# Kernel tuning notes

Measured on AMD Instinct MI355X. Metric: run time of the kernel, lower is better.

## Reference

```python
import jax, jax.numpy as jnp
import numpy as np

N, E, D, F = 8192, 262144, 256, 512  # nodes, edges, hidden_dim, ffn hidden
M = 256  # performer num_random_features (default)


def _ln(x, g, b, eps=1e-5):
    mu = jnp.mean(x, axis=-1, keepdims=True)
    var = jnp.mean((x - mu) ** 2, axis=-1, keepdims=True)
    return (x - mu) * jax.lax.rsqrt(var + eps) * g + b


def setup_inputs() -> dict:
    key = jax.random.key(0)
    ks = jax.random.split(key, 16)
    s = 1.0 / np.sqrt(D)
    return {
        "h": jax.random.normal(ks[0], (N, D), dtype=jnp.float32),
        "edge_index": jax.random.randint(ks[1], (2, E), 0, N, dtype=jnp.int32),
        "W_gcn": jax.random.normal(ks[2], (D, D), dtype=jnp.float32) * s,
        "b_gcn": jnp.zeros((D,), jnp.float32),
        "Wq": jax.random.normal(ks[3], (D, D), dtype=jnp.float32) * s,
        "bq": jnp.zeros((D,), jnp.float32),
        "Wk": jax.random.normal(ks[4], (D, D), dtype=jnp.float32) * s,
        "bk": jnp.zeros((D,), jnp.float32),
        "Wv": jax.random.normal(ks[5], (D, D), dtype=jnp.float32) * s,
        "bv": jnp.zeros((D,), jnp.float32),
        "Wo": jax.random.normal(ks[6], (D, D), dtype=jnp.float32) * s,
        "bo": jnp.zeros((D,), jnp.float32),
        "RF": jax.random.normal(ks[7], (M, D), dtype=jnp.float32) * s,  # random feature projection
        "g1": jnp.ones((D,), jnp.float32), "be1": jnp.zeros((D,), jnp.float32),
        "g2": jnp.ones((D,), jnp.float32), "be2": jnp.zeros((D,), jnp.float32),
        "g3": jnp.ones((D,), jnp.float32), "be3": jnp.zeros((D,), jnp.float32),
        "W1": jax.random.normal(ks[8], (D, F), dtype=jnp.float32) * s,
        "b1": jnp.zeros((F,), jnp.float32),
        "W2": jax.random.normal(ks[9], (F, D), dtype=jnp.float32) * (1.0 / np.sqrt(F)),
        "b2": jnp.zeros((D,), jnp.float32),
    }


def _gps_forward(h, edge_index, W_gcn, b_gcn, Wq, bq, Wk, bk, Wv, bv, Wo, bo, RF,
                 g1, be1, g2, be2, g3, be3, W1, b1, W2, b2):
    n = h.shape[0]
    # ---- local GCNConv (add self loops, symmetric norm) ----
    loops = jnp.arange(n, dtype=edge_index.dtype)
    src = jnp.concatenate([edge_index[0], loops])
    dst = jnp.concatenate([edge_index[1], loops])
    deg = jax.ops.segment_sum(jnp.ones_like(src, dtype=h.dtype), dst, num_segments=n)
    dinv = jnp.where(deg > 0, jax.lax.rsqrt(jnp.maximum(deg, 1e-12)), 0.0)
    coef = dinv[src] * dinv[dst]  # [E+N]
    xw = h @ W_gcn  # [N, D]
    h_local = jax.ops.segment_sum(xw[src] * coef[:, None], dst, num_segments=n) + b_gcn
    h1 = _ln(h + h_local, g1, be1)  # dropout p applied in train only; eval here
    # ---- global Performer attention (as written: dense NxN in feature space) ----
    q = h1 @ Wq + bq
    k = h1 @ Wk + bk
    v = h1 @ Wv + bv
    qf = q @ RF.T  # [N, M]
    kf = k @ RF.T  # [N, M]
    scores = (qf @ kf.T) / jnp.sqrt(jnp.asarray(h.shape[-1], h.dtype))  # [N, N]
    attw = jax.nn.softmax(scores, axis=-1)
    h_global = (attw @ v) @ Wo + bo
    h2 = _ln(h1 + h_global, g2, be2)
    # ---- FFN ----
    h_ffn = jnp.maximum(h2 @ W1 + b1, 0.0) @ W2 + b2
    return _ln(h2 + h_ffn, g3, be3)


def reference(h, edge_index, W_gcn, b_gcn, Wq, bq, Wk, bk, Wv, bv, Wo, bo, RF,
              g1, be1, g2, be2, g3, be3, W1, b1, W2, b2):
    return _gps_forward(h, edge_index, W_gcn, b_gcn, Wq, bq, Wk, bk, Wv, bv, Wo, bo, RF,
                        g1, be1, g2, be2, g3, be3, W1, b1, W2, b2)
```

## Files before the change

### kernel.cpp

```cpp
#include <hip/hip_runtime.h>
#include <hip/hip_bf16.h>

#define NN 8192
#define EE 262144
#define DD 256
#define FF 512
#define MM 256

typedef __attribute__((ext_vector_type(8))) short short8v;
typedef __attribute__((ext_vector_type(16))) float float16v;

__device__ __forceinline__ ushort f2bf(float x) {
  union { float f; unsigned u; } c; c.f = x;
  unsigned r = (c.u + 0x7FFF + ((c.u >> 16) & 1)) >> 16;
  return (ushort)r;
}
__device__ __forceinline__ float b2f(ushort u) {
  union { unsigned u; float f; } c; c.u = ((unsigned)u) << 16;
  return c.f;
}
__device__ __forceinline__ void async_copy16(void* lds, const void* g) {
  __builtin_amdgcn_global_load_lds(
      (const __attribute__((address_space(1))) void*)g,
      (__attribute__((address_space(3))) void*)lds, 16, 0, 0);
}

__global__ __launch_bounds__(1024) void scan_kernel(const int* __restrict__ degi,
                                                    int* __restrict__ csr_off,
                                                    float* __restrict__ dinv) {
  __shared__ int part[1024];
  int tid = threadIdx.x;
  int base = tid * 8;
  int loc[8], dv[8]; int s = 0;
#pragma unroll
  for (int i = 0; i < 8; ++i) { int d = degi[base + i]; dv[i] = d; loc[i] = s; s += d; }
  part[tid] = s;
  __syncthreads();
  for (int off = 1; off < 1024; off <<= 1) {
    int v = (tid >= off) ? part[tid - off] : 0;
    __syncthreads();
    part[tid] += v;
    __syncthreads();
  }
  int pre = (tid == 0) ? 0 : part[tid - 1];
#pragma unroll
  for (int i = 0; i < 8; ++i) {
    csr_off[base + i] = pre + loc[i];
    dinv[base + i] = rsqrtf((float)(dv[i] + 1));
  }
  if (tid == 1023) csr_off[NN] = part[1023];
}

__global__ void fill_kernel(const int* __restrict__ ei, const int* __restrict__ csr_off,
                            int* __restrict__ cursor, int* __restrict__ csr_src) {
  int i = blockIdx.x * blockDim.x + threadIdx.x;
  if (i < EE) {
    int d = ei[EE + i];
    int pos = csr_off[d] + atomicAdd(&cursor[d], 1);
    csr_src[pos] = ei[i];
  }
}

#define QSCALE 0.090168441f
#define P1B 10753
__global__ __launch_bounds__(256) void prep_kernel(
    const float* __restrict__ h, const float* __restrict__ W_gcn,
    const float* __restrict__ Wv, const float* __restrict__ Wo,
    const float* __restrict__ W1, const float* __restrict__ W2,
    const float* __restrict__ bv,
    const float* __restrict__ Wq, const float* __restrict__ Wk,
    const float* __restrict__ bq, const float* __restrict__ bk,
    const float* __restrict__ RF, const int* __restrict__ ei,
    ushort* __restrict__ hb, ushort* __restrict__ WgcnT, ushort* __restrict__ Wcat,
    ushort* __restrict__ WoT, ushort* __restrict__ W1T, ushort* __restrict__ W2T,
    ushort* __restrict__ RFb, ushort* __restrict__ Wqkb,
    float* __restrict__ bcat, int* __restrict__ degi)
{
  if (blockIdx.x < P1B) {
    int i = blockIdx.x * 256 + threadIdx.x;
    const int R0 = NN * DD;
    const int R1 = R0 + DD * DD;
    const int R2 = R1 + DD * DD;
    const int R3 = R2 + DD * DD;
    const int R4 = R3 + DD * FF;
    const int R5 = R4 + FF * DD;
    const int R6 = R5 + DD;
    const int R7 = R6 + DD * DD;
    const int R8 = R7 + DD * DD;
    const int R9 = R8 + DD * DD;
    if (i < R0) {
      hb[i] = f2bf(h[i]);
    } else if (i < R1) {
      int j = i - R0; int n = j >> 8, k = j & 255;
      WgcnT[(n << 8) | k] = f2bf(W_gcn[k * DD + n]);
    } else if (i < R2) {
      int j = i - R1; int n = j >> 8, k = j & 255;
      Wcat[((512 + n) << 8) | k] = f2bf(Wv[k * DD + n]);
    } else if (i < R3) {
      int j = i - R2; int n = j >> 8, k = j & 255;
      WoT[(n << 8) | k] = f2bf(Wo[k * DD + n]);
    } else if (i < R4) {
      int j = i - R3; int n = j >> 8, k = j & 255;
      W1T[(n << 8) | k] = f2bf(W1[k * FF + n]);
    } else if (i < R5) {
      int j = i - R4; int n = j >> 9, k = j & 511;
      W2T[n * FF + k] = f2bf(W2[k * DD + n]);
    } else if (i < R6) {
      bcat[512 + (i - R5)] = bv[i - R5];
    } else if (i < R7) {
      int j = i - R6;
      RFb[j] = f2bf(RF[j]);
    } else if (i < R8) {
      int j = i - R7;
      Wqkb[j] = f2bf(Wq[j] * QSCALE);
    } else if (i < R9) {
      int j = i - R8;
      Wqkb[DD * DD + j] = f2bf(Wk[j]);
    }
  } else if (blockIdx.x < P1B + 2) {
    const int b = blockIdx.x - P1B;
    const int m = threadIdx.x;
    const float* bvec = (b == 0) ? bq : bk;
    const float alpha = (b == 0) ? QSCALE : 1.0f;
    float s = 0.0f;
    for (int j = 0; j < DD; ++j) s = fmaf(bvec[j], RF[m * DD + j], s);
    bcat[(b == 0 ? 0 : 256) + m] = s * alpha;
  } else {
    int i = (blockIdx.x - P1B - 2) * 256 + threadIdx.x;
    if (i < EE) atomicAdd(&degi[ei[EE + i]], 1);
  }
}

template<int OMODE, bool RELU>
__global__ __launch_bounds__(512) void gemm_bf16_kernel(
    const ushort* __restrict__ A, const ushort* __restrict__ BT,
    const float* __restrict__ bias, void* __restrict__ Cv,
    void* __restrict__ Cv2, void* __restrict__ Cv3,
    int M, int N, int K)
{
  __shared__ ushort As[2][4096];
  __shared__ ushort Bs[2][4096];
  const int tid = threadIdx.x;
  const int c32 = tid & 31, hi = (tid >> 5) & 1;
  const int wv = tid >> 6;
  const int q = wv & 3, ks = wv >> 2;
  const int qm = (q >> 1) << 5, qn = (q & 1) << 5;
  const int m0 = blockIdx.y * 64, n0 = blockIdx.x * 64;

  const int sr = tid >> 3, spsl = tid & 7;
  const int ssl = spsl ^ ((sr >> 2) & 7);
  const ushort* Asrc = A + (size_t)(m0 + sr) * K + (ssl << 3);
  const ushort* Bsrc = BT + (size_t)(n0 + sr) * K + (ssl << 3);

  const int ra = qm + c32, rb = qn + c32;
  const int ga = (ra >> 2) & 7, gb = (rb >> 2) & 7;

  float16v acc = (float16v)(0.0f);

#define GS(b, k0) { \
    async_copy16(&As[b][tid << 3], Asrc + (k0)); \
    async_copy16(&Bs[b][tid << 3], Bsrc + (k0)); }

  GS(0, 0)
  const int nk = K >> 6;
  for (int kt = 0; kt < nk; ++kt) {
    asm volatile("s_waitcnt vmcnt(0)" ::: "memory");
    __syncthreads();
    if (kt + 1 < nk) GS((kt + 1) & 1, (kt + 1) << 6)
    const ushort* as_ = As[kt & 1];
    const ushort* bs_ = Bs[kt & 1];
    __builtin_amdgcn_s_setprio(1);
#pragma unroll
    for (int k2 = 0; k2 < 2; ++k2) {
      const int k16 = (ks << 1) + k2;
      const int sl = (k16 << 1) + hi;
      short8v af = *(const short8v*)&as_[(ra << 6) + ((sl ^ ga) << 3)];
      short8v bf = *(const short8v*)&bs_[(rb << 6) + ((sl ^ gb) << 3)];
      acc = __builtin_amdgcn_mfma_f32_32x32x16_bf16(af, bf, acc, 0, 0, 0);
    }
    __builtin_amdgcn_s_setprio(0);
  }
#undef GS

  __syncthreads();
  float* red = (float*)&As[0][0];
  if (ks == 1) {
#pragma unroll
    for (int r = 0; r < 16; ++r) {
      const int crow = (r & 3) + ((r >> 2) << 3) + (hi << 2);
      red[(q << 10) + (crow << 5) + c32] = acc[r];
    }
  }
  __syncthreads();
  if (ks == 0) {
    const int col = n0 + qn + c32;
    const float bv = bias ? bias[col] : 0.0f;
    if (OMODE == 3 && col >= 512) {
#pragma unroll
      for (int g = 0; g < 4; ++g) {
        float v0 = acc[g * 4 + 0] + red[(q << 10) + (((0) + (g << 3) + (hi << 2)) << 5) + c32] + bv;
        float v1 = acc[g * 4 + 1] + red[(q << 10) + (((1) + (g << 3) + (hi << 2)) << 5) + c32] + bv;
        float v2 = acc[g * 4 + 2] + red[(q << 10) + (((2) + (g << 3) + (hi << 2)) << 5) + c32] + bv;
        float v3 = acc[g * 4 + 3] + red[(q << 10) + (((3) + (g << 3) + (hi << 2)) << 5) + c32] + bv;
        ushort4 o; o.x = f2bf(v0); o.y = f2bf(v1); o.z = f2bf(v2); o.w = f2bf(v3);
        *(ushort4*)&((ushort*)Cv3)[(size_t)(col - 512) * NN + m0 + qm + (g << 3) + (hi << 2)] = o;
      }
    } else {
#pragma unroll
      for (int r = 0; r < 16; ++r) {
        const int crow = (r & 3) + ((r >> 2) << 3) + (hi << 2);
        const int m = m0 + qm + crow;
        float v = acc[r] + red[(q << 10) + (crow << 5) + c32] + bv;
        if (RELU) v = fmaxf(v, 0.0f);
        if (OMODE == 4) {
          ((ushort*)Cv)[(size_t)m * N + col] = f2bf(v);
        } else if (OMODE == 5) {
          if (col < 256) ((ushort*)Cv)[(size_t)m * 256 + col] = f2bf(v);
          else ((ushort*)Cv)[(size_t)(256 + m) * 256 + (col - 256)] = f2bf(v);
        } else {
          if (col < 256) {
            ((ushort*)Cv)[(size_t)m * 256 + col] = f2bf(v);
          } else {
            const int c2 = (col - 256) ^ ((m & 7) << 3) ^ (((m >> 3) & 3) << 6);
            ((ushort*)Cv2)[(size_t)m * 256 + c2] = f2bf(v);
          }
        }
      }
    }
  }
}

__global__ __launch_bounds__(256) void gcn_gather_ln_kernel(
    const ushort* __restrict__ xwb, const float* __restrict__ h,
    const float* __restrict__ dinv, const int* __restrict__ csr_off,
    const int* __restrict__ csr_src, const float* __restrict__ b_gcn,
    const float* __restrict__ g1, const float* __restrict__ be1,
    float* __restrict__ h1, ushort* __restrict__ h1b)
{
  const int node = blockIdx.x * 4 + (threadIdx.x >> 6);
  const int t = threadIdx.x & 63;
  const int c4 = t << 2;
  const float di = dinv[node];
  const int e0 = csr_off[node], e1 = csr_off[node + 1];
  float acc[4] = {0.f, 0.f, 0.f, 0.f};
  for (int e = e0; e < e1; ++e) {
    int s = csr_src[e];
    float ds = dinv[s];
    ushort4 xv = *(const ushort4*)&xwb[(size_t)s * DD + c4];
    acc[0] = fmaf(b2f(xv.x), ds, acc[0]);
    acc[1] = fmaf(b2f(xv.y), ds, acc[1]);
    acc[2] = fmaf(b2f(xv.z), ds, acc[2]);
    acc[3] = fmaf(b2f(xv.w), ds, acc[3]);
  }
  ushort4 sv = *(const ushort4*)&xwb[(size_t)node * DD + c4];
  float4 hv = *(const float4*)&h[(size_t)node * DD + c4];
  float4 bg = *(const float4*)&b_gcn[c4];
  const float dii = di * di;
  float y[4];
  y[0] = fmaf(acc[0], di, b2f(sv.x) * dii) + bg.x + hv.x;
  y[1] = fmaf(acc[1], di, b2f(sv.y) * dii) + bg.y + hv.y;
  y[2] = fmaf(acc[2], di, b2f(sv.z) * dii) + bg.z + hv.z;
  y[3] = fmaf(acc[3], di, b2f(sv.w) * dii) + bg.w + hv.w;
  float s1 = (y[0] + y[1]) + (y[2] + y[3]);
  float s2 = (y[0]*y[0] + y[1]*y[1]) + (y[2]*y[2] + y[3]*y[3]);
#pragma unroll
  for (int m = 1; m <= 32; m <<= 1) { s1 += __shfl_xor(s1, m); s2 += __shfl_xor(s2, m); }
  float mu = s1 * (1.0f / 256.0f);
  float var = s2 * (1.0f / 256.0f) - mu * mu;
  float inv = rsqrtf(fmaxf(var, 0.0f) + 1e-5f);
  float4 g4 = *(const float4*)&g1[c4];
  float4 b4 = *(const float4*)&be1[c4];
  float v0 = (y[0] - mu) * inv * g4.x + b4.x;
  float v1 = (y[1] - mu) * inv * g4.y + b4.y;
  float v2 = (y[2] - mu) * inv * g4.z + b4.z;
  float v3 = (y[3] - mu) * inv * g4.w + b4.w;
  *(float4*)&h1[(size_t)node * DD + c4] = make_float4(v0, v1, v2, v3);
  ushort4 ob; ob.x = f2bf(v0); ob.y = f2bf(v1); ob.z = f2bf(v2); ob.w = f2bf(v3);
  *(ushort4*)&h1b[(node << 8) + c4] = ob;
}

__global__ __launch_bounds__(256, 2) void flash_mfma_kernel(
    const ushort* __restrict__ qb, const ushort* __restrict__ kb,
    const ushort* __restrict__ vbT, ushort* __restrict__ opb,
    float* __restrict__ ml, int ksn, int kchunk)
{
  __shared__ ushort Kbuf[2][8192];
  __shared__ ushort Vbuf[2][8192];

  const int tid = threadIdx.x;
  const int l = tid & 63, wv = tid >> 6;
  const int c32 = l & 31, hi = l >> 5;
  const int qt = blockIdx.x / ksn, ks = blockIdx.x % ksn;
  const int q0 = qt * 128;
  const int kbase = ks * kchunk;

  const int vrow = tid >> 2;
  const ushort* kptr = kb + (size_t)(kbase + (tid >> 5)) * 256 + ((tid & 31) << 3);
  const ushort* vptr = vbT + (size_t)vrow * NN + kbase + (((tid & 3) ^ ((vrow >> 3) & 3)) << 3);

#define FSTAGE(b) { \
    _Pragma("unroll") \
    for (int c = 0; c < 4; ++c) { \
      async_copy16(&Kbuf[b][((c << 8) + tid) << 3], kptr + (size_t)c * (8 * 256)); \
      async_copy16(&Vbuf[b][((c << 8) + tid) << 3], vptr + (size_t)c * (64 * NN)); \
    } }

  FSTAGE(0)

  short8v qfr[16];
  {
    const ushort* qrow = qb + (size_t)(q0 + wv * 32 + c32) * 256 + (hi << 3);
#pragma unroll
    for (int kk = 0; kk < 16; ++kk)
      qfr[kk] = *(const short8v*)(qrow + (kk << 4));
  }

  float16v acc[8];
#pragma unroll
  for (int dt = 0; dt < 8; ++dt) acc[dt] = (float16v)(0.0f);
  float lsum = 0.f;

  const int ksw = ((c32 & 7) << 3) | (((c32 >> 3) & 3) << 6);
  const int vsw = (c32 >> 3) & 3;
  const int voff0 = (hi ^ vsw) << 3;
  const int voff1 = ((2 + hi) ^ vsw) << 3;

  const int nit = kchunk >> 5;
  for (int it = 0; it < nit; ++it) {
    asm volatile("s_waitcnt vmcnt(0)" ::: "memory");
    __syncthreads();
    if (it + 1 < nit) {
      kptr += 32 * 256;
      vptr += 32;
      FSTAGE((it + 1) & 1)
    }
    const ushort* Kp = Kbuf[it & 1];
    const ushort* Vp = Vbuf[it & 1];

    float16v s = (float16v)(0.0f);
    __builtin_amdgcn_s_setprio(1);
#pragma unroll
    for (int kk = 0; kk < 16; ++kk) {
      short8v kf = *(const short8v*)&Kp[(c32 << 8) + (((kk << 4) + (hi << 3)) ^ ksw)];
      s = __builtin_amdgcn_mfma_f32_32x32x16_bf16(kf, qfr[kk], s, 0, 0, 0);
    }
    __builtin_amdgcn_s_setprio(0);

    float p[16];
#pragma unroll
    for (int r = 0; r < 16; ++r) p[r] = exp2f(s[r]);
    {
      float t0 = (p[0] + p[1]) + (p[2] + p[3]);
      float t1 = (p[4] + p[5]) + (p[6] + p[7]);
      float t2 = (p[8] + p[9]) + (p[10] + p[11]);
      float t3 = (p[12] + p[13]) + (p[14] + p[15]);
      lsum += (t0 + t1) + (t2 + t3);
    }
    unsigned u0, u1, u2, u3, u4, u5, u6, u7;
    asm("v_cvt_pk_bf16_f32 %0, %1, %2" : "=v"(u0) : "v"(p[0]),  "v"(p[1]));
    asm("v_cvt_pk_bf16_f32 %0, %1, %2" : "=v"(u1) : "v"(p[2]),  "v"(p[3]));
    asm("v_cvt_pk_bf16_f32 %0, %1, %2" : "=v"(u2) : "v"(p[4]),  "v"(p[5]));
    asm("v_cvt_pk_bf16_f32 %0, %1, %2" : "=v"(u3) : "v"(p[6]),  "v"(p[7]));
    asm("v_cvt_pk_bf16_f32 %0, %1, %2" : "=v"(u4) : "v"(p[8]),  "v"(p[9]));
    asm("v_cvt_pk_bf16_f32 %0, %1, %2" : "=v"(u5) : "v"(p[10]), "v"(p[11]));
    asm("v_cvt_pk_bf16_f32 %0, %1, %2" : "=v"(u6) : "v"(p[12]), "v"(p[13]));
    asm("v_cvt_pk_bf16_f32 %0, %1, %2" : "=v"(u7) : "v"(p[14]), "v"(p[15]));
    asm volatile("v_permlane32_swap_b32 %0, %1" : "+v"(u0), "+v"(u2));
    asm volatile("v_permlane32_swap_b32 %0, %1" : "+v"(u1), "+v"(u3));
    asm volatile("v_permlane32_swap_b32 %0, %1" : "+v"(u4), "+v"(u6));
    asm volatile("v_permlane32_swap_b32 %0, %1" : "+v"(u5), "+v"(u7));
    union { unsigned uu[4]; short8v v; } P0, P1;
    P0.uu[0] = u0; P0.uu[1] = u1; P0.uu[2] = u2; P0.uu[3] = u3;
    P1.uu[0] = u4; P1.uu[1] = u5; P1.uu[2] = u6; P1.uu[3] = u7;

    __builtin_amdgcn_s_setprio(1);
#pragma unroll
    for (int dt = 0; dt < 8; ++dt) {
      const int drow = (dt << 5) + c32;
      short8v vf0 = *(const short8v*)&Vp[(drow << 5) + voff0];
      short8v vf1 = *(const short8v*)&Vp[(drow << 5) + voff1];
      acc[dt] = __builtin_amdgcn_mfma_f32_32x32x16_bf16(P0.v, vf0, acc[dt], 0, 0, 0);
      acc[dt] = __builtin_amdgcn_mfma_f32_32x32x16_bf16(P1.v, vf1, acc[dt], 0, 0, 0);
    }
    __builtin_amdgcn_s_setprio(0);
  }
#undef FSTAGE

  float lt = lsum + __shfl_xor(lsum, 32);
  if (hi == 0) ml[(size_t)ks * NN + q0 + wv * 32 + c32] = lt;
  ushort* op = opb + (size_t)ks * (NN * DD);
#pragma unroll
  for (int dt = 0; dt < 8; ++dt)
#pragma unroll
    for (int r = 0; r < 16; ++r) {
      const int qrow = q0 + wv * 32 + (r & 3) + ((r >> 2) << 3) + (hi << 2);
      op[(size_t)qrow * DD + (dt << 5) + c32] = f2bf(acc[dt][r]);
    }
}

__global__ __launch_bounds__(256) void flash_merge_kernel(
    const ushort* __restrict__ opb, const float* __restrict__ ml,
    ushort* __restrict__ hgb, int ksn)
{
  const int t = threadIdx.x;
  const int row = blockIdx.x * 8 + (t >> 5);
  const int cg = t & 31;
  float num[8] = {0.f, 0.f, 0.f, 0.f, 0.f, 0.f, 0.f, 0.f};
  float L = 0.f;
  for (int i = 0; i < ksn; ++i) {
    L += ml[(size_t)i * NN + row];
    short8v v = *(const short8v*)&opb[(size_t)i * NN * DD + (size_t)row * DD + (cg << 3)];
#pragma unroll
    for (int j = 0; j < 8; ++j) num[j] += b2f((ushort)v[j]);
  }
  float inv = 1.0f / L;
  short8v o;
#pragma unroll
  for (int j = 0; j < 8; ++j) o[j] = (short)f2bf(num[j] * inv);
  *(short8v*)&hgb[(row << 8) + (cg << 3)] = o;
}

__global__ __launch_bounds__(512, 4) void epilogue_kernel(
    const ushort* __restrict__ hgb, const float* __restrict__ h1,
    const ushort* __restrict__ WoT, const float* __restrict__ bo,
    const float* __restrict__ g2, const float* __restrict__ be2,
    const ushort* __restrict__ W1T, const float* __restrict__ b1,
    const ushort* __restrict__ W2T, const float* __restrict__ b2,
    const float* __restrict__ g3, const float* __restrict__ be3,
    float* __restrict__ out)
{
  __shared__ float  yL[32 * 256];
  __shared__ ushort h2bL[32 * 256];
  __shared__ ushort tL[32 * 512];

  const int tid = threadIdx.x;
  const int c32 = tid & 31, hi = (tid >> 5) & 1;
  const int wv = tid >> 6;
  const int lane = tid & 63;
  const int m0 = blockIdx.x * 32;
  const int n0 = wv << 5;
  const int col = n0 + c32;

  float16v acc = (float16v)(0.0f);
#pragma unroll
  for (int k0 = 0; k0 < 256; k0 += 16) {
    short8v af = *(const short8v*)&hgb[(size_t)(m0 + c32) * 256 + k0 + (hi << 3)];
    short8v bf = *(const short8v*)&WoT[(size_t)col * 256 + k0 + (hi << 3)];
    acc = __builtin_amdgcn_mfma_f32_32x32x16_bf16(af, bf, acc, 0, 0, 0);
  }
  {
    const float bov = bo[col];
#pragma unroll
    for (int r = 0; r < 16; ++r) {
      const int row = (r & 3) + ((r >> 2) << 3) + (hi << 2);
      yL[(row << 8) + col] = acc[r] + bov + h1[(size_t)(m0 + row) * 256 + col];
    }
  }
  __syncthreads();
#pragma unroll
  for (int rr = 0; rr < 4; ++rr) {
    const int row = (wv << 2) + rr;
    const int c4 = lane << 2;
    float4 v = *(const float4*)&yL[(row << 8) + c4];
    float s1 = (v.x + v.y) + (v.z + v.w);
    float s2 = (v.x * v.x + v.y * v.y) + (v.z * v.z + v.w * v.w);
#pragma unroll
    for (int m = 1; m <= 32; m <<= 1) { s1 += __shfl_xor(s1, m); s2 += __shfl_xor(s2, m); }
    float mu = s1 * (1.0f / 256.0f);
    float var = s2 * (1.0f / 256.0f) - mu * mu;
    float inv = rsqrtf(fmaxf(var, 0.0f) + 1e-5f);
    float4 g4 = *(const float4*)&g2[c4];
    float4 b4 = *(const float4*)&be2[c4];
    float o0 = (v.x - mu) * inv * g4.x + b4.x;
    float o1 = (v.y - mu) * inv * g4.y + b4.y;
    float o2 = (v.z - mu) * inv * g4.z + b4.z;
    float o3 = (v.w - mu) * inv * g4.w + b4.w;
    *(float4*)&yL[(row << 8) + c4] = make_float4(o0, o1, o2, o3);
    const int psl = (c4 >> 3) ^ (row & 7);
    ushort4 ob; ob.x = f2bf(o0); ob.y = f2bf(o1); ob.z = f2bf(o2); ob.w = f2bf(o3);
    *(ushort4*)&h2bL[(row << 8) + (psl << 3) + (c4 & 7)] = ob;
  }
  __syncthreads();
  {
    float16v a1[2] = {(float16v)(0.0f), (float16v)(0.0f)};
    const int f0 = wv << 6;
#pragma unroll
    for (int k0 = 0; k0 < 256; k0 += 16) {
      const int s = (k0 >> 3) + hi;
      short8v af = *(const short8v*)&h2bL[(c32 << 8) + ((s ^ (c32 & 7)) << 3)];
#pragma unroll
      for (int nt = 0; nt < 2; ++nt) {
        short8v bf = *(const short8v*)&W1T[(size_t)(f0 + (nt << 5) + c32) * 256 + k0 + (hi << 3)];
        a1[nt] = __builtin_amdgcn_mfma_f32_32x32x16_bf16(af, bf, a1[nt], 0, 0, 0);
      }
    }
#pragma unroll
    for (int nt = 0; nt < 2; ++nt) {
      const int col1 = f0 + (nt << 5) + c32;
      const float b1v = b1[col1];
#pragma unroll
      for (int r = 0; r < 16; ++r) {
        const int row = (r & 3) + ((r >> 2) << 3) + (hi << 2);
        float v = fmaxf(a1[nt][r] + b1v, 0.0f);
        const int psl = (col1 >> 3) ^ (row & 7);
        tL[(row << 9) + (psl << 3) + (col1 & 7)] = f2bf(v);
      }
    }
  }
  __syncthreads();
  float16v a2 = (float16v)(0.0f);
#pragma unroll
  for (int k0 = 0; k0 < 512; k0 += 16) {
    const int s = (k0 >> 3) + hi;
    short8v af = *(const short8v*)&tL[(c32 << 9) + ((s ^ (c32 & 7)) << 3)];
    short8v bf = *(const short8v*)&W2T[(size_t)col * 512 + k0 + (hi << 3)];
    a2 = __builtin_amdgcn_mfma_f32_32x32x16_bf16(af, bf, a2, 0, 0, 0);
  }
  {
    const float b2v = b2[col];
#pragma unroll
    for (int r = 0; r < 16; ++r) {
      const int row = (r & 3) + ((r >> 2) << 3) + (hi << 2);
      a2[r] += b2v + yL[(row << 8) + col];
    }
  }
  __syncthreads();
  {
    float* y2L = (float*)tL;
#pragma unroll
    for (int r = 0; r < 16; ++r) {
      const int row = (r & 3) + ((r >> 2) << 3) + (hi << 2);
      y2L[(row << 8) + col] = a2[r];
    }
  }
  __syncthreads();
  {
    const float* y2L = (const float*)tL;
#pragma unroll
    for (int rr = 0; rr < 4; ++rr) {
      const int row = (wv << 2) + rr;
      const int c4 = lane << 2;
      float4 v = *(const float4*)&y2L[(row << 8) + c4];
      float s1 = (v.x + v.y) + (v.z + v.w);
      float s2 = (v.x * v.x + v.y * v.y) + (v.z * v.z + v.w * v.w);
#pragma unroll
      for (int m = 1; m <= 32; m <<= 1) { s1 += __shfl_xor(s1, m); s2 += __shfl_xor(s2, m); }
      float mu = s1 * (1.0f / 256.0f);
      float var = s2 * (1.0f / 256.0f) - mu * mu;
      float inv = rsqrtf(fmaxf(var, 0.0f) + 1e-5f);
      float4 g4 = *(const float4*)&g3[c4];
      float4 b4 = *(const float4*)&be3[c4];
      float4 o;
      o.x = (v.x - mu) * inv * g4.x + b4.x;
      o.y = (v.y - mu) * inv * g4.y + b4.y;
      o.z = (v.z - mu) * inv * g4.z + b4.z;
      o.w = (v.w - mu) * inv * g4.w + b4.w;
      *(float4*)&out[(size_t)(m0 + row) * 256 + c4] = o;
    }
  }
}

extern "C" void kernel_launch(void* const* d_in, const int* in_sizes, int n_in,
                              void* d_out, int out_size, void* d_ws, size_t ws_size,
                              hipStream_t stream) {
  (void)in_sizes; (void)n_in; (void)out_size;
  const float* h     = (const float*)d_in[0];
  const int*   ei    = (const int*)  d_in[1];
  const float* W_gcn = (const float*)d_in[2];
  const float* b_gcn = (const float*)d_in[3];
  const float* Wq    = (const float*)d_in[4];
  const float* bq    = (const float*)d_in[5];
  const float* Wk    = (const float*)d_in[6];
  const float* bk    = (const float*)d_in[7];
  const float* Wv    = (const float*)d_in[8];
  const float* bv    = (const float*)d_in[9];
  const float* Wo    = (const float*)d_in[10];
  const float* bo    = (const float*)d_in[11];
  const float* RF    = (const float*)d_in[12];
  const float* g1    = (const float*)d_in[13];
  const float* be1   = (const float*)d_in[14];
  const float* g2    = (const float*)d_in[15];
  const float* be2   = (const float*)d_in[16];
  const float* g3    = (const float*)d_in[17];
  const float* be3   = (const float*)d_in[18];
  const float* W1    = (const float*)d_in[19];
  const float* b1    = (const float*)d_in[20];
  const float* W2    = (const float*)d_in[21];
  const float* b2    = (const float*)d_in[22];
  float* out = (float*)d_out;

  const size_t M2 = (size_t)NN * DD;
  const int ksn = (ws_size >= (size_t)64 * 1024 * 1024) ? 8 : 4;
  const int kchunk = NN / ksn;

  char* base = (char*)d_ws;
  float*  h1   = (float*)base;  base += M2 * 4;
  ushort* hbX  = (ushort*)base; base += M2 * 2;
  ushort* h1bX = (ushort*)base; base += M2 * 2;
  ushort* qb   = (ushort*)base; base += M2 * 2;
  ushort* kb   = (ushort*)base; base += M2 * 2;
  ushort* vbT  = (ushort*)base; base += M2 * 2;
  ushort* opb  = (ushort*)base;
  float*  R    = (float*)opb;   base += (size_t)ksn * M2 * 2;
  float*  mlf  = (float*)base;  base += (size_t)8 * NN * 4;
  ushort* WgcnT = (ushort*)base; base += DD * DD * 2;
  ushort* Wcat  = (ushort*)base; base += (size_t)768 * DD * 2;
  ushort* WoT   = (ushort*)base; base += DD * DD * 2;
  ushort* W1T   = (ushort*)base; base += FF * DD * 2;
  ushort* W2T   = (ushort*)base; base += DD * FF * 2;
  ushort* RFb   = (ushort*)base; base += DD * DD * 2;
  ushort* Wqkb  = (ushort*)base; base += (size_t)2 * DD * DD * 2;
  float*  bcat  = (float*)base;  base += 768 * 4;
  float*  dinv  = (float*)base;  base += NN * 4;
  int* degi    = (int*)base; base += NN * 4;
  int* cursor  = (int*)base; base += NN * 4;
  int* csr_off = (int*)base; base += (NN + 4) * 4;
  int* csr_src = (int*)base; base += EE * 4;

  ushort* xwb = (ushort*)R;
  ushort* hgb = hbX;

  hipMemsetAsync(degi, 0, (size_t)2 * NN * sizeof(int), stream);

  prep_kernel<<<P1B + 2 + 1024, 256, 0, stream>>>(
      h, W_gcn, Wv, Wo, W1, W2, bv, Wq, Wk, bq, bk, RF, ei,
      hbX, WgcnT, Wcat, WoT, W1T, W2T, RFb, Wqkb, bcat, degi);

  scan_kernel<<<1, 1024, 0, stream>>>(degi, csr_off, dinv);
  fill_kernel<<<EE / 256, 256, 0, stream>>>(ei, csr_off, cursor, csr_src);

  gemm_bf16_kernel<5, false><<<dim3(8, 4), 512, 0, stream>>>(
      RFb, Wqkb, nullptr, Wcat, nullptr, nullptr, DD, 512, DD);

  gemm_bf16_kernel<4, false><<<dim3(DD / 64, NN / 64), 512, 0, stream>>>(
      hbX, WgcnT, nullptr, xwb, nullptr, nullptr, NN, DD, DD);
  gcn_gather_ln_kernel<<<NN / 4, 256, 0, stream>>>(xwb, h, dinv, csr_off, csr_src, b_gcn, g1, be1, h1, h1bX);
  gemm_bf16_kernel<3, false><<<dim3(768 / 64, NN / 64), 512, 0, stream>>>(
      h1bX, Wcat, bcat, qb, kb, vbT, NN, 768, DD);
  flash_mfma_kernel<<<(NN / 128) * ksn, 256, 0, stream>>>(qb, kb, vbT, opb, mlf, ksn, kchunk);
  flash_merge_kernel<<<NN / 8, 256, 0, stream>>>(opb, mlf, hgb, ksn);
  epilogue_kernel<<<NN / 32, 512, 0, stream>>>(
      hgb, h1, WoT, bo, g2, be2, W1T, b1, W2T, b2, g3, be3, out);
}
```

Measured before the change: 215.6 us.

## Fuse flash merge into epilogue, merge weight-prep and XW GEMMs, drop fp32 h1

The split-K flash merge (sum partial outputs, divide by L) now runs at the start of the epilogue kernel and writes into swizzled LDS instead of a global bf16 buffer. The two small GEMMs (RF·Wq/Wk fold and h·W_gcn) become one launch that picks its role from the block index. The fp32 h1 residual is dropped and the bf16 copy is used instead. This removes two launches and several global round trips, at the cost of bf16 precision in the LN2 residual and an extra sync plus per-block merge work in the epilogue.

```diff
diff --git a/kernel.cpp b/kernel.cpp
--- a/kernel.cpp
+++ b/kernel.cpp
@@ -135,7 +135,7 @@
 __global__ __launch_bounds__(512) void gemm_bf16_kernel(
     const ushort* __restrict__ A, const ushort* __restrict__ BT,
     const float* __restrict__ bias, void* __restrict__ Cv,
-    void* __restrict__ Cv2, void* __restrict__ Cv3,
+    void* __restrict__ Cv2, void* __restrict__ Cv3, void* __restrict__ Cv4,
     int M, int N, int K)
 {
   __shared__ ushort As[2][4096];
@@ -145,12 +145,27 @@
   const int wv = tid >> 6;
   const int q = wv & 3, ks = wv >> 2;
   const int qm = (q >> 1) << 5, qn = (q & 1) << 5;
-  const int m0 = blockIdx.y * 64, n0 = blockIdx.x * 64;
+
+  const ushort* pA = A;
+  const ushort* pBT = BT;
+  int m0 = blockIdx.y * 64;
+  const int n0 = blockIdx.x * 64;
+  bool xw_path = true;
+  if (OMODE == 6) {
+    if (blockIdx.y < 128) {
+      if (blockIdx.x >= 4) return;
+    } else {
+      xw_path = false;
+      pA = (const ushort*)Cv2;
+      pBT = (const ushort*)Cv3;
+      m0 = (blockIdx.y - 128) * 64;
+    }
+  }
 
   const int sr = tid >> 3, spsl = tid & 7;
   const int ssl = spsl ^ ((sr >> 2) & 7);
-  const ushort* Asrc = A + (size_t)(m0 + sr) * K + (ssl << 3);
-  const ushort* Bsrc = BT + (size_t)(n0 + sr) * K + (ssl << 3);
+  const ushort* Asrc = pA + (size_t)(m0 + sr) * K + (ssl << 3);
+  const ushort* Bsrc = pBT + (size_t)(n0 + sr) * K + (ssl << 3);
 
   const int ra = qm + c32, rb = qn + c32;
   const int ga = (ra >> 2) & 7, gb = (rb >> 2) & 7;
@@ -214,9 +229,14 @@
         if (RELU) v = fmaxf(v, 0.0f);
         if (OMODE == 4) {
           ((ushort*)Cv)[(size_t)m * N + col] = f2bf(v);
-        } else if (OMODE == 5) {
-          if (col < 256) ((ushort*)Cv)[(size_t)m * 256 + col] = f2bf(v);
-          else ((ushort*)Cv)[(size_t)(256 + m) * 256 + (col - 256)] = f2bf(v);
+        } else if (OMODE == 6) {
+          if (xw_path) {
+            ((ushort*)Cv)[(size_t)m * 256 + col] = f2bf(v);
+          } else {
+            ushort* W = (ushort*)Cv4;
+            if (col < 256) W[(size_t)m * 256 + col] = f2bf(v);
+            else W[(size_t)(256 + m) * 256 + (col - 256)] = f2bf(v);
+          }
         } else {
           if (col < 256) {
             ((ushort*)Cv)[(size_t)m * 256 + col] = f2bf(v);
@@ -235,7 +255,7 @@
     const float* __restrict__ dinv, const int* __restrict__ csr_off,
     const int* __restrict__ csr_src, const float* __restrict__ b_gcn,
     const float* __restrict__ g1, const float* __restrict__ be1,
-    float* __restrict__ h1, ushort* __restrict__ h1b)
+    ushort* __restrict__ h1b)
 {
   const int node = blockIdx.x * 4 + (threadIdx.x >> 6);
   const int t = threadIdx.x & 63;
@@ -274,7 +294,6 @@
   float v1 = (y[1] - mu) * inv * g4.y + b4.y;
   float v2 = (y[2] - mu) * inv * g4.z + b4.z;
   float v3 = (y[3] - mu) * inv * g4.w + b4.w;
-  *(float4*)&h1[(size_t)node * DD + c4] = make_float4(v0, v1, v2, v3);
   ushort4 ob; ob.x = f2bf(v0); ob.y = f2bf(v1); ob.z = f2bf(v2); ob.w = f2bf(v3);
   *(ushort4*)&h1b[(node << 8) + c4] = ob;
 }
@@ -398,40 +417,21 @@
     }
 }
 
-__global__ __launch_bounds__(256) void flash_merge_kernel(
+__global__ __launch_bounds__(512, 4) void epilogue_kernel(
     const ushort* __restrict__ opb, const float* __restrict__ ml,
-    ushort* __restrict__ hgb, int ksn)
-{
-  const int t = threadIdx.x;
-  const int row = blockIdx.x * 8 + (t >> 5);
-  const int cg = t & 31;
-  float num[8] = {0.f, 0.f, 0.f, 0.f, 0.f, 0.f, 0.f, 0.f};
-  float L = 0.f;
-  for (int i = 0; i < ksn; ++i) {
-    L += ml[(size_t)i * NN + row];
-    short8v v = *(const short8v*)&opb[(size_t)i * NN * DD + (size_t)row * DD + (cg << 3)];
-#pragma unroll
-    for (int j = 0; j < 8; ++j) num[j] += b2f((ushort)v[j]);
-  }
-  float inv = 1.0f / L;
-  short8v o;
-#pragma unroll
-  for (int j = 0; j < 8; ++j) o[j] = (short)f2bf(num[j] * inv);
-  *(short8v*)&hgb[(row << 8) + (cg << 3)] = o;
-}
-
-__global__ __launch_bounds__(512, 4) void epilogue_kernel(
-    const ushort* __restrict__ hgb, const float* __restrict__ h1,
+    const ushort* __restrict__ h1b,
     const ushort* __restrict__ WoT, const float* __restrict__ bo,
     const float* __restrict__ g2, const float* __restrict__ be2,
     const ushort* __restrict__ W1T, const float* __restrict__ b1,
     const ushort* __restrict__ W2T, const float* __restrict__ b2,
     const float* __restrict__ g3, const float* __restrict__ be3,
-    float* __restrict__ out)
+    float* __restrict__ out, int ksn)
 {
   __shared__ float  yL[32 * 256];
   __shared__ ushort h2bL[32 * 256];
   __shared__ ushort tL[32 * 512];
+
+  ushort* hgL = tL;
 
   const int tid = threadIdx.x;
   const int c32 = tid & 31, hi = (tid >> 5) & 1;
@@ -441,19 +441,56 @@
   const int n0 = wv << 5;
   const int col = n0 + c32;
 
+  {
+    const int row = tid >> 4;
+    const int cseg = (tid & 15) << 4;
+    const int growp = m0 + row;
+    float L = 0.f;
+    for (int i = 0; i < ksn; ++i) L += ml[(size_t)i * NN + growp];
+    const float invl = 1.0f / L;
+    float num[16];
+#pragma unroll
+    for (int j = 0; j < 16; ++j) num[j] = 0.f;
+    for (int i = 0; i < ksn; ++i) {
+      const ushort* src = opb + (size_t)i * ((size_t)NN * DD) + (size_t)growp * DD + cseg;
+      short8v v0 = *(const short8v*)src;
+      short8v v1 = *(const short8v*)(src + 8);
+#pragma unroll
+      for (int j = 0; j < 8; ++j) {
+        num[j]     += b2f((ushort)v0[j]);
+        num[8 + j] += b2f((ushort)v1[j]);
+      }
+    }
+    const int swz = (row & 7) ^ (((row >> 3) & 3) << 3);
+    const int sl0 = (cseg >> 3);
+    union { ushort us[8]; short8v v; } o0, o1;
+#pragma unroll
+    for (int j = 0; j < 8; ++j) {
+      o0.us[j] = f2bf(num[j] * invl);
+      o1.us[j] = f2bf(num[8 + j] * invl);
+    }
+    *(short8v*)&hgL[(row << 8) + ((sl0 ^ swz) << 3)] = o0.v;
+    *(short8v*)&hgL[(row << 8) + (((sl0 + 1) ^ swz) << 3)] = o1.v;
+  }
+  __syncthreads();
+
   float16v acc = (float16v)(0.0f);
-#pragma unroll
-  for (int k0 = 0; k0 < 256; k0 += 16) {
-    short8v af = *(const short8v*)&hgb[(size_t)(m0 + c32) * 256 + k0 + (hi << 3)];
-    short8v bf = *(const short8v*)&WoT[(size_t)col * 256 + k0 + (hi << 3)];
-    acc = __builtin_amdgcn_mfma_f32_32x32x16_bf16(af, bf, acc, 0, 0, 0);
+  {
+    const int aswz = (c32 & 7) ^ (((c32 >> 3) & 3) << 3);
+#pragma unroll
+    for (int k0 = 0; k0 < 256; k0 += 16) {
+      const int sA = (k0 >> 3) + hi;
+      short8v af = *(const short8v*)&hgL[(c32 << 8) + ((sA ^ aswz) << 3)];
+      short8v bf = *(const short8v*)&WoT[(size_t)col * 256 + k0 + (hi << 3)];
+      acc = __builtin_amdgcn_mfma_f32_32x32x16_bf16(af, bf, acc, 0, 0, 0);
+    }
   }
   {
     const float bov = bo[col];
 #pragma unroll
     for (int r = 0; r < 16; ++r) {
       const int row = (r & 3) + ((r >> 2) << 3) + (hi << 2);
-      yL[(row << 8) + col] = acc[r] + bov + h1[(size_t)(m0 + row) * 256 + col];
+      yL[(row << 8) + col] = acc[r] + bov + b2f(h1b[(size_t)(m0 + row) * 256 + col]);
     }
   }
   __syncthreads();
@@ -594,7 +631,6 @@
   const int kchunk = NN / ksn;
 
   char* base = (char*)d_ws;
-  float*  h1   = (float*)base;  base += M2 * 4;
   ushort* hbX  = (ushort*)base; base += M2 * 2;
   ushort* h1bX = (ushort*)base; base += M2 * 2;
   ushort* qb   = (ushort*)base; base += M2 * 2;
@@ -618,7 +654,6 @@
   int* csr_src = (int*)base; base += EE * 4;
 
   ushort* xwb = (ushort*)R;
-  ushort* hgb = hbX;
 
   hipMemsetAsync(degi, 0, (size_t)2 * NN * sizeof(int), stream);
 
@@ -626,19 +661,16 @@
       h, W_gcn, Wv, Wo, W1, W2, bv, Wq, Wk, bq, bk, RF, ei,
       hbX, WgcnT, Wcat, WoT, W1T, W2T, RFb, Wqkb, bcat, degi);
 
+  gemm_bf16_kernel<6, false><<<dim3(8, 132), 512, 0, stream>>>(
+      hbX, WgcnT, nullptr, xwb, RFb, Wqkb, Wcat, NN, DD, DD);
+
   scan_kernel<<<1, 1024, 0, stream>>>(degi, csr_off, dinv);
   fill_kernel<<<EE / 256, 256, 0, stream>>>(ei, csr_off, cursor, csr_src);
 
-  gemm_bf16_kernel<5, false><<<dim3(8, 4), 512, 0, stream>>>(
-      RFb, Wqkb, nullptr, Wcat, nullptr, nullptr, DD, 512, DD);
-
-  gemm_bf16_kernel<4, false><<<dim3(DD / 64, NN / 64), 512, 0, stream>>>(
-      hbX, WgcnT, nullptr, xwb, nullptr, nullptr, NN, DD, DD);
-  gcn_gather_ln_kernel<<<NN / 4, 256, 0, stream>>>(xwb, h, dinv, csr_off, csr_src, b_gcn, g1, be1, h1, h1bX);
+  gcn_gather_ln_kernel<<<NN / 4, 256, 0, stream>>>(xwb, h, dinv, csr_off, csr_src, b_gcn, g1, be1, h1bX);
   gemm_bf16_kernel<3, false><<<dim3(768 / 64, NN / 64), 512, 0, stream>>>(
-      h1bX, Wcat, bcat, qb, kb, vbT, NN, 768, DD);
+      h1bX, Wcat, bcat, qb, kb, vbT, nullptr, NN, 768, DD);
   flash_mfma_kernel<<<(NN / 128) * ksn, 256, 0, stream>>>(qb, kb, vbT, opb, mlf, ksn, kchunk);
-  flash_merge_kernel<<<NN / 8, 256, 0, stream>>>(opb, mlf, hgb, ksn);
   epilogue_kernel<<<NN / 32, 512, 0, stream>>>(
-      hgb, h1, WoT, bo, g2, be2, W1T, b1, W2T, b2, g3, be3, out);
-}
+      opb, mlf, h1bX, WoT, bo, g2, be2, W1T, b1, W2T, b2, g3, be3, out, ksn);
+}
```

New measurement: 212.6 us. Within noise of the previous version (-1.4%).
